# Performance work log

Hardware: AMD Instinct MI355X
Metric: run time of the kernel (lower is better)

## Reference

```python
import jax, jax.numpy as jnp
import numpy as np

N, IN_CH, HID, HEADS, OUT_CH, E = 30000, 256, 128, 4, 256, 480000
NEG_SLOPE = 0.2  # PyG GATConv default LeakyReLU slope


def setup_inputs() -> dict:
    key = jax.random.key(0)
    ks = jax.random.split(key, 12)
    s = lambda fin: 1.0 / np.sqrt(fin)
    return {
        "x": jax.random.normal(ks[0], (N, IN_CH), jnp.float32),
        "edge_index": jax.random.randint(ks[1], (2, E), 0, N, jnp.int32),
        "W1": jax.random.normal(ks[2], (IN_CH, HEADS * HID), jnp.float32) * s(IN_CH),
        "a_src1": jax.random.normal(ks[3], (HEADS, HID), jnp.float32) * s(HID),
        "a_dst1": jax.random.normal(ks[4], (HEADS, HID), jnp.float32) * s(HID),
        "b1": jnp.zeros((HEADS * HID,), jnp.float32),
        "prelu_w": jnp.asarray(0.25, jnp.float32),
        "W2": jax.random.normal(ks[5], (HEADS * HID, OUT_CH), jnp.float32) * s(HEADS * HID),
        "a_src2": jax.random.normal(ks[6], (1, OUT_CH), jnp.float32) * s(OUT_CH),
        "a_dst2": jax.random.normal(ks[7], (1, OUT_CH), jnp.float32) * s(OUT_CH),
        "b2": jnp.zeros((OUT_CH,), jnp.float32),
    }


def gat_conv(x, W, a_src, a_dst, bias, src, dst, heads, out_ch, concat):
    n = x.shape[0]
    h = (x @ W).reshape(n, heads, out_ch)                 # [n,H,C]
    al_s = jnp.einsum("nhc,hc->nh", h, a_src)             # [n,H]
    al_d = jnp.einsum("nhc,hc->nh", h, a_dst)
    logits = jax.nn.leaky_relu(al_s[src] + al_d[dst], NEG_SLOPE)  # [Et,H]
    m = jax.lax.stop_gradient(jax.ops.segment_max(logits, dst, num_segments=n))
    e = jnp.exp(logits - m[dst])
    denom = jax.ops.segment_sum(e, dst, num_segments=n)
    alpha = e / denom[dst]                                # per-dst softmax
    msg = h[src] * alpha[:, :, None]                      # [Et,H,C]
    out = jax.ops.segment_sum(msg, dst, num_segments=n)   # [n,H,C]
    out = out.reshape(n, heads * out_ch) if concat else out.mean(axis=1)
    return out + bias


def reference(x, edge_index, W1, a_src1, a_dst1, b1, prelu_w, W2, a_src2, a_dst2, b2):
    n = x.shape[0]
    loop = jnp.arange(n, dtype=edge_index.dtype)
    src = jnp.concatenate([edge_index[0], loop])          # PyG adds self-loops
    dst = jnp.concatenate([edge_index[1], loop])
    h = gat_conv(x, W1, a_src1, a_dst1, b1, src, dst, HEADS, HID, concat=True)
    h = jnp.where(h >= 0, h, prelu_w * h)                 # PReLU (eval: dropout off)
    z = gat_conv(h, W2, a_src2, a_dst2, b2, src, dst, 1, OUT_CH, concat=False)
    return z
```

## Files before the change

kernel.cpp:

```cpp
#include <hip/hip_runtime.h>
#include <hip/hip_bf16.h>
#include <float.h>

#define N_NODES 30000
#define IN_CH   256
#define HID     128
#define HEADS   4
#define OUT_CH  256
#define N_EDGES 480000
#define TOT_E   (N_EDGES + N_NODES)

typedef unsigned short u16;
typedef __attribute__((ext_vector_type(8))) unsigned short u16x8;
typedef __attribute__((ext_vector_type(8))) short          s16x8;
typedef __attribute__((ext_vector_type(4))) float          f32x4;

__device__ inline float bf2f(u16 u) {
    union { unsigned int i; float f; } v; v.i = ((unsigned int)u) << 16; return v.f;
}
__device__ inline u16 f2bf(float f) {
    union { float f; unsigned int i; } u; u.f = f;
    unsigned int r = u.i + 0x7FFF + ((u.i >> 16) & 1);
    return (u16)(r >> 16);
}

__global__ void detect_k(const unsigned int* __restrict__ w, int* __restrict__ flag) {
    __shared__ int votes;
    if (threadIdx.x == 0) votes = 0;
    __syncthreads();
    int v = 0;
    for (int i = threadIdx.x; i < 2048; i += 256) {
        unsigned int e = (w[i] >> 7) & 0xFFu;
        if (e >= 100u && e <= 140u) v++;
    }
    atomicAdd(&votes, v);
    __syncthreads();
    if (threadIdx.x == 0) *flag = (votes > 1024) ? 1 : 0;
}

__global__ void convert_bf_k(const void* __restrict__ in, u16* __restrict__ out,
                             int n, const int* __restrict__ flag) {
    int i = blockIdx.x * blockDim.x + threadIdx.x;
    if (i >= n) return;
    if (*flag) out[i] = ((const u16*)in)[i];
    else       out[i] = f2bf(((const float*)in)[i]);
}

__global__ void convert_tr_k(const void* __restrict__ in, u16* __restrict__ out,
                             int rows, int cols, const int* __restrict__ flag) {
    int i = blockIdx.x * blockDim.x + threadIdx.x;
    if (i >= rows * cols) return;
    int r = i / cols, c = i - r * cols;
    u16 v = (*flag) ? ((const u16*)in)[i] : f2bf(((const float*)in)[i]);
    out[(size_t)c * rows + r] = v;
}

__global__ void convert_small_k(const void* __restrict__ as1, const void* __restrict__ ad1,
                                const void* __restrict__ b1,  const void* __restrict__ as2,
                                const void* __restrict__ ad2, const void* __restrict__ b2,
                                const void* __restrict__ pw,
                                float* __restrict__ as1f, float* __restrict__ ad1f,
                                float* __restrict__ b1f,  float* __restrict__ as2f,
                                float* __restrict__ ad2f, float* __restrict__ b2f,
                                float* __restrict__ pwf,
                                const int* __restrict__ flag)
{
    int i = blockIdx.x * blockDim.x + threadIdx.x;
    int f = *flag;
#define CV(in, k) (f ? bf2f(((const u16*)(in))[k]) : ((const float*)(in))[k])
    if      (i < 512)  as1f[i]        = CV(as1, i);
    else if (i < 1024) ad1f[i - 512]  = CV(ad1, i - 512);
    else if (i < 1536) b1f [i - 1024] = CV(b1,  i - 1024);
    else if (i < 1792) as2f[i - 1536] = CV(as2, i - 1536);
    else if (i < 2048) ad2f[i - 1792] = CV(ad2, i - 1792);
    else if (i < 2304) b2f [i - 2048] = CV(b2,  i - 2048);
    else if (i == 2304) pwf[0]        = CV(pw, 0);
#undef CV
}

__global__ __launch_bounds__(256) void prep_av_k(
    const u16* __restrict__ W1t, const float* __restrict__ as1f,
    const float* __restrict__ ad1f, float* __restrict__ vsd)
{
    int idx = blockIdx.x * 256 + threadIdx.x;
    if (idx >= 2048) return;
    int v = idx >> 8;
    int k = idx & 255;
    int h = v & 3;
    const float* av = (v < 4) ? as1f : ad1f;
    float s = 0.f;
    for (int c = 0; c < 128; ++c)
        s += bf2f(W1t[(size_t)(h*128 + c)*256 + k]) * av[h*128 + c];
    vsd[idx] = s;
}

__global__ __launch_bounds__(64) void logits1_k(
    const u16* __restrict__ xb, const float* __restrict__ vsd,
    float* __restrict__ als, float* __restrict__ ald)
{
    int n = blockIdx.x, lane = threadIdx.x;
    int c0 = lane * 4;
    ushort4 xv = *(const ushort4*)(xb + (size_t)n*IN_CH + c0);
    float x0 = bf2f(xv.x), x1 = bf2f(xv.y), x2 = bf2f(xv.z), x3 = bf2f(xv.w);
#pragma unroll
    for (int v = 0; v < 8; ++v) {
        float4 vv = *(const float4*)(vsd + v*256 + c0);
        float d = x0*vv.x + x1*vv.y + x2*vv.z + x3*vv.w;
#pragma unroll
        for (int o = 32; o > 0; o >>= 1) d += __shfl_xor(d, o);
        if (lane == 0) {
            if (v < 4) als[(size_t)n*4 + v]     = d;
            else       ald[(size_t)n*4 + v - 4] = d;
        }
    }
}

__global__ __launch_bounds__(256) void gemm_bf_k(const u16* __restrict__ A,
                                                 const u16* __restrict__ Bt,
                                                 u16* __restrict__ Cb,
                                                 const float* __restrict__ a_s,
                                                 const float* __restrict__ a_d,
                                                 float* __restrict__ als,
                                                 float* __restrict__ ald,
                                                 int M, int N, int K,
                                                 int H, int hshift)
{
    __shared__ __align__(16) u16 As[128][40];
    __shared__ __align__(16) u16 Bs[128][40];

    const int tid  = threadIdx.x;
    const int wid  = tid >> 6;
    const int lane = tid & 63;
    const int wr   = wid >> 1;
    const int wc   = wid & 1;
    const int lr   = lane & 15;
    const int lg   = lane >> 4;
    const int row0 = blockIdx.y * 128;
    const int col0 = blockIdx.x * 128;

    const int st_r = tid >> 1;
    const int st_c = (tid & 1) << 4;

    f32x4 acc[4][4];
#pragma unroll
    for (int i = 0; i < 4; ++i)
#pragma unroll
        for (int j = 0; j < 4; ++j)
            acc[i][j] = (f32x4){0.f, 0.f, 0.f, 0.f};

    for (int k0 = 0; k0 < K; k0 += 32) {
        __syncthreads();
        {
            u16x8 a0 = {}, a1 = {};
            int ar = row0 + st_r;
            if (ar < M) {
                const u16* ap = A + (size_t)ar * K + k0 + st_c;
                a0 = *(const u16x8*)ap;
                a1 = *(const u16x8*)(ap + 8);
            }
            *(u16x8*)&As[st_r][st_c]     = a0;
            *(u16x8*)&As[st_r][st_c + 8] = a1;
            const u16* bp = Bt + (size_t)(col0 + st_r) * K + k0 + st_c;
            *(u16x8*)&Bs[st_r][st_c]     = *(const u16x8*)bp;
            *(u16x8*)&Bs[st_r][st_c + 8] = *(const u16x8*)(bp + 8);
        }
        __syncthreads();

        s16x8 af[4], bf[4];
#pragma unroll
        for (int mf = 0; mf < 4; ++mf)
            af[mf] = *(const s16x8*)&As[wr*64 + mf*16 + lr][lg*8];
#pragma unroll
        for (int nf = 0; nf < 4; ++nf)
            bf[nf] = *(const s16x8*)&Bs[wc*64 + nf*16 + lr][lg*8];
#pragma unroll
        for (int mf = 0; mf < 4; ++mf)
#pragma unroll
            for (int nf = 0; nf < 4; ++nf)
                acc[mf][nf] = __builtin_amdgcn_mfma_f32_16x16x32_bf16(
                    af[mf], bf[nf], acc[mf][nf], 0, 0, 0);
    }

    const int head = (col0 + wc*64) >> hshift;
    float asj[4], adj[4];
#pragma unroll
    for (int nf = 0; nf < 4; ++nf) {
        int j = col0 + wc*64 + nf*16 + lr;
        asj[nf] = a_s[j];
        adj[nf] = a_d[j];
    }
#pragma unroll
    for (int mf = 0; mf < 4; ++mf) {
#pragma unroll
        for (int r = 0; r < 4; ++r) {
            int rr = row0 + wr*64 + mf*16 + lg*4 + r;
            float ss = 0.f, sd = 0.f;
#pragma unroll
            for (int nf = 0; nf < 4; ++nf) {
                float v = acc[mf][nf][r];
                ss += v * asj[nf];
                sd += v * adj[nf];
            }
#pragma unroll
            for (int m2 = 1; m2 < 16; m2 <<= 1) {
                ss += __shfl_xor(ss, m2);
                sd += __shfl_xor(sd, m2);
            }
            if (rr < M) {
                if (lr == 0) {
                    atomicAdd(&als[(size_t)rr * H + head], ss);
                    atomicAdd(&ald[(size_t)rr * H + head], sd);
                }
                size_t base = (size_t)rr * N + col0 + wc*64 + lr;
#pragma unroll
                for (int nf = 0; nf < 4; ++nf)
                    Cb[base + nf*16] = f2bf(acc[mf][nf][r]);
            }
        }
    }
}

__global__ __launch_bounds__(256) void gemm_h1_k(const u16* __restrict__ A,
                                                 const u16* __restrict__ Bt,
                                                 u16* __restrict__ Cb,
                                                 const float* __restrict__ bias,
                                                 const float* __restrict__ prelu_w,
                                                 int M)
{
    __shared__ __align__(16) u16 As[128][40];
    __shared__ __align__(16) u16 Bs[128][40];

    const int h    = blockIdx.z;
    const int tid  = threadIdx.x;
    const int wid  = tid >> 6;
    const int lane = tid & 63;
    const int wr   = wid >> 1;
    const int wc   = wid & 1;
    const int lr   = lane & 15;
    const int lg   = lane >> 4;
    const int row0 = blockIdx.y * 128;

    const int st_r = tid >> 1;
    const int st_c = (tid & 1) << 4;

    f32x4 acc[4][4];
#pragma unroll
    for (int i = 0; i < 4; ++i)
#pragma unroll
        for (int j = 0; j < 4; ++j)
            acc[i][j] = (f32x4){0.f, 0.f, 0.f, 0.f};

    for (int k0 = 0; k0 < 256; k0 += 32) {
        __syncthreads();
        {
            u16x8 a0 = {}, a1 = {};
            int ar = row0 + st_r;
            if (ar < M) {
                const u16* ap = A + (size_t)ar * 1024 + h*256 + k0 + st_c;
                a0 = *(const u16x8*)ap;
                a1 = *(const u16x8*)(ap + 8);
            }
            *(u16x8*)&As[st_r][st_c]     = a0;
            *(u16x8*)&As[st_r][st_c + 8] = a1;
            const u16* bp = Bt + (size_t)(h*128 + st_r) * 256 + k0 + st_c;
            *(u16x8*)&Bs[st_r][st_c]     = *(const u16x8*)bp;
            *(u16x8*)&Bs[st_r][st_c + 8] = *(const u16x8*)(bp + 8);
        }
        __syncthreads();

        s16x8 af[4], bf[4];
#pragma unroll
        for (int mf = 0; mf < 4; ++mf)
            af[mf] = *(const s16x8*)&As[wr*64 + mf*16 + lr][lg*8];
#pragma unroll
        for (int nf = 0; nf < 4; ++nf)
            bf[nf] = *(const s16x8*)&Bs[wc*64 + nf*16 + lr][lg*8];
#pragma unroll
        for (int mf = 0; mf < 4; ++mf)
#pragma unroll
            for (int nf = 0; nf < 4; ++nf)
                acc[mf][nf] = __builtin_amdgcn_mfma_f32_16x16x32_bf16(
                    af[mf], bf[nf], acc[mf][nf], 0, 0, 0);
    }

    const float pw = *prelu_w;
#pragma unroll
    for (int mf = 0; mf < 4; ++mf) {
#pragma unroll
        for (int r = 0; r < 4; ++r) {
            int rr = row0 + wr*64 + mf*16 + lg*4 + r;
            if (rr >= M) continue;
            size_t base = (size_t)rr * 512 + h*128 + wc*64 + lr;
#pragma unroll
            for (int nf = 0; nf < 4; ++nf) {
                int j = wc*64 + nf*16 + lr;
                float v = acc[mf][nf][r] + bias[h*128 + j];
                v = (v >= 0.f) ? v : pw * v;
                Cb[base + nf*16] = f2bf(v);
            }
        }
    }
}

__global__ void zero_k(int* p, int n) {
    int i = blockIdx.x*blockDim.x + threadIdx.x; if (i < n) p[i] = 0;
}
__global__ void count_k(const int* __restrict__ ei, int* __restrict__ cnt) {
    int i = blockIdx.x*blockDim.x + threadIdx.x;
    if (i >= TOT_E) return;
    int d = (i < N_EDGES) ? ei[N_EDGES + i] : (i - N_EDGES);
    atomicAdd(&cnt[d], 1);
}
__global__ __launch_bounds__(1024) void scan1_k(const int* __restrict__ cnt,
                                                int* __restrict__ offs,
                                                int* __restrict__ btot)
{
    __shared__ int sm[1024];
    int tid = threadIdx.x;
    int i = blockIdx.x * 1024 + tid;
    int v = (i < N_NODES) ? cnt[i] : 0;
    sm[tid] = v;
    __syncthreads();
    for (int off = 1; off < 1024; off <<= 1) {
        int t = (tid >= off) ? sm[tid - off] : 0;
        __syncthreads();
        sm[tid] += t;
        __syncthreads();
    }
    if (i < N_NODES) offs[i + 1] = sm[tid];
    if (tid == 1023) btot[blockIdx.x] = sm[1023];
}
__global__ void scan2_k(const int* __restrict__ btot, int* __restrict__ bpref, int nb)
{
    int lane = threadIdx.x;
    int orig = (lane < nb) ? btot[lane] : 0;
    int v = orig;
    for (int off = 1; off < 64; off <<= 1) {
        int t = __shfl_up(v, off);
        if (lane >= off) v += t;
    }
    if (lane < nb) bpref[lane] = v - orig;
}
__global__ __launch_bounds__(1024) void scan3_k(const int* __restrict__ cnt,
                                                int* __restrict__ offs,
                                                int* __restrict__ cursor,
                                                const int* __restrict__ bpref)
{
    int i = blockIdx.x * 1024 + threadIdx.x;
    if (i < N_NODES) {
        int inc = offs[i + 1] + bpref[blockIdx.x];
        offs[i + 1] = inc;
        cursor[i]   = inc - cnt[i];
    }
    if (i == 0) offs[0] = 0;
}
__global__ void scatter_k(const int* __restrict__ ei, int* __restrict__ cursor,
                          int* __restrict__ ssrc)
{
    int i = blockIdx.x*blockDim.x + threadIdx.x;
    if (i >= TOT_E) return;
    int s, d;
    if (i < N_EDGES) { s = ei[i]; d = ei[N_EDGES + i]; }
    else             { s = i - N_EDGES; d = s; }
    int pos = atomicAdd(&cursor[d], 1);
    ssrc[pos] = s;
}

__global__ __launch_bounds__(64) void aggx_k(
    const u16* __restrict__ xb,
    const float* __restrict__ als,
    const float* __restrict__ ald,
    const int* __restrict__ offs,
    const int* __restrict__ ssrc,
    u16* __restrict__ aggx)
{
    const int n = blockIdx.x, tid = threadIdx.x;
    const int beg = offs[n], end = offs[n+1];

    float aldh[4];
#pragma unroll
    for (int h = 0; h < 4; ++h) aldh[h] = ald[(size_t)n*4 + h];

    float lsum[4] = {0.f, 0.f, 0.f, 0.f};
    for (int e = beg + tid; e < end; e += 64) {
        int s = ssrc[e];
        float4 a = *(const float4*)(als + (size_t)s*4);
        float la[4] = {a.x, a.y, a.z, a.w};
#pragma unroll
        for (int h = 0; h < 4; ++h) {
            float l = la[h] + aldh[h];
            l = (l >= 0.f) ? l : 0.2f*l;
            lsum[h] += __expf(l);
        }
    }
#pragma unroll
    for (int h = 0; h < 4; ++h)
#pragma unroll
        for (int o = 32; o > 0; o >>= 1) lsum[h] += __shfl_xor(lsum[h], o);
    float inv[4];
#pragma unroll
    for (int h = 0; h < 4; ++h) inv[h] = 1.0f / lsum[h];

    __shared__ int    sh_s[64];
    __shared__ float4 sh_w[64];
    const int c0 = tid * 4;
    float acc[4][4] = {};
    for (int chunk = beg; chunk < end; chunk += 64) {
        int e = chunk + tid;
        if (e < end) {
            int s = ssrc[e];
            sh_s[tid] = s;
            float4 a = *(const float4*)(als + (size_t)s*4);
            float la[4] = {a.x, a.y, a.z, a.w};
            float wv[4];
#pragma unroll
            for (int h = 0; h < 4; ++h) {
                float l = la[h] + aldh[h];
                l = (l >= 0.f) ? l : 0.2f*l;
                wv[h] = __expf(l) * inv[h];
            }
            sh_w[tid] = make_float4(wv[0], wv[1], wv[2], wv[3]);
        }
        __syncthreads();
        int cnt = min(64, end - chunk);
        int j = 0;
        for (; j + 4 <= cnt; j += 4) {
            int s0 = sh_s[j+0], s1 = sh_s[j+1], s2 = sh_s[j+2], s3 = sh_s[j+3];
            float4 w0 = sh_w[j+0], w1 = sh_w[j+1], w2 = sh_w[j+2], w3 = sh_w[j+3];
            ushort4 v0 = *(const ushort4*)(xb + (size_t)s0*IN_CH + c0);
            ushort4 v1 = *(const ushort4*)(xb + (size_t)s1*IN_CH + c0);
            ushort4 v2 = *(const ushort4*)(xb + (size_t)s2*IN_CH + c0);
            ushort4 v3 = *(const ushort4*)(xb + (size_t)s3*IN_CH + c0);
            float x0[4] = {bf2f(v0.x), bf2f(v0.y), bf2f(v0.z), bf2f(v0.w)};
            float x1[4] = {bf2f(v1.x), bf2f(v1.y), bf2f(v1.z), bf2f(v1.w)};
            float x2[4] = {bf2f(v2.x), bf2f(v2.y), bf2f(v2.z), bf2f(v2.w)};
            float x3[4] = {bf2f(v3.x), bf2f(v3.y), bf2f(v3.z), bf2f(v3.w)};
            float wa0[4] = {w0.x, w0.y, w0.z, w0.w};
            float wa1[4] = {w1.x, w1.y, w1.z, w1.w};
            float wa2[4] = {w2.x, w2.y, w2.z, w2.w};
            float wa3[4] = {w3.x, w3.y, w3.z, w3.w};
#pragma unroll
            for (int h = 0; h < 4; ++h)
#pragma unroll
                for (int k = 0; k < 4; ++k)
                    acc[h][k] += wa0[h]*x0[k] + wa1[h]*x1[k]
                               + wa2[h]*x2[k] + wa3[h]*x3[k];
        }
        for (; j < cnt; ++j) {
            int s0 = sh_s[j];
            float4 w0 = sh_w[j];
            ushort4 v0 = *(const ushort4*)(xb + (size_t)s0*IN_CH + c0);
            float x0[4] = {bf2f(v0.x), bf2f(v0.y), bf2f(v0.z), bf2f(v0.w)};
            float wa[4] = {w0.x, w0.y, w0.z, w0.w};
#pragma unroll
            for (int h = 0; h < 4; ++h)
#pragma unroll
                for (int k = 0; k < 4; ++k)
                    acc[h][k] += wa[h]*x0[k];
        }
        __syncthreads();
    }

    u16* op = aggx + (size_t)n * 1024;
#pragma unroll
    for (int h = 0; h < 4; ++h) {
        ushort4 o;
        o.x = f2bf(acc[h][0]); o.y = f2bf(acc[h][1]);
        o.z = f2bf(acc[h][2]); o.w = f2bf(acc[h][3]);
        *(ushort4*)(op + h*256 + c0) = o;
    }
}

template<int H, int C, int VW, bool PRELU, int OUTMODE>
__global__ __launch_bounds__(64) void aggregate_k(
    const u16* __restrict__ hb,
    const float* __restrict__ als,
    const float* __restrict__ ald,
    const int* __restrict__ offs,
    const int* __restrict__ ssrc,
    const float* __restrict__ bias,
    const float* __restrict__ prelu_w,
    void* __restrict__ outv,
    const int* __restrict__ flag)
{
    constexpr int CT = H * C;
    constexpr int T  = 64;
    static_assert(CT == T * VW, "geometry");
    const int n   = blockIdx.x;
    const int tid = threadIdx.x;
    const int beg = offs[n], end = offs[n+1];

    float aldh[H];
#pragma unroll
    for (int h = 0; h < H; ++h) aldh[h] = ald[(size_t)n*H + h];

    float lsum[H];
#pragma unroll
    for (int h = 0; h < H; ++h) lsum[h] = 0.f;
    for (int e = beg + tid; e < end; e += T) {
        int s = ssrc[e];
#pragma unroll
        for (int h = 0; h < H; ++h) {
            float l = als[(size_t)s*H + h] + aldh[h];
            l = (l >= 0.f) ? l : 0.2f*l;
            lsum[h] += __expf(l);
        }
    }
#pragma unroll
    for (int h = 0; h < H; ++h) {
#pragma unroll
        for (int o = 32; o > 0; o >>= 1) lsum[h] += __shfl_xor(lsum[h], o);
    }
    float inv[H];
#pragma unroll
    for (int h = 0; h < H; ++h) inv[h] = 1.0f / lsum[h];

    __shared__ int   sh_s[T];
    __shared__ float sh_w[H][T];
    const int hh = (VW * tid) / C;
    float acc[VW];
#pragma unroll
    for (int k = 0; k < VW; ++k) acc[k] = 0.f;

    for (int chunk = beg; chunk < end; chunk += T) {
        int e = chunk + tid;
        if (e < end) {
            int s = ssrc[e];
            sh_s[tid] = s;
#pragma unroll
            for (int h = 0; h < H; ++h) {
                float l = als[(size_t)s*H + h] + aldh[h];
                l = (l >= 0.f) ? l : 0.2f*l;
                sh_w[h][tid] = __expf(l) * inv[h];
            }
        }
        __syncthreads();
        int cnt = min(T, end - chunk);
        int j = 0;
        for (; j + 4 <= cnt; j += 4) {
            int   s0 = sh_s[j+0], s1 = sh_s[j+1], s2 = sh_s[j+2], s3 = sh_s[j+3];
            float w0 = sh_w[hh][j+0], w1 = sh_w[hh][j+1];
            float w2 = sh_w[hh][j+2], w3 = sh_w[hh][j+3];
            if constexpr (VW == 8) {
                u16x8 v0 = *(const u16x8*)(hb + (size_t)s0*CT + VW*tid);
                u16x8 v1 = *(const u16x8*)(hb + (size_t)s1*CT + VW*tid);
                u16x8 v2 = *(const u16x8*)(hb + (size_t)s2*CT + VW*tid);
                u16x8 v3 = *(const u16x8*)(hb + (size_t)s3*CT + VW*tid);
#pragma unroll
                for (int k = 0; k < 8; ++k) {
                    acc[k] += w0*bf2f(v0[k]) + w1*bf2f(v1[k])
                            + w2*bf2f(v2[k]) + w3*bf2f(v3[k]);
                }
            } else {
                ushort4 v0 = *(const ushort4*)(hb + (size_t)s0*CT + VW*tid);
                ushort4 v1 = *(const ushort4*)(hb + (size_t)s1*CT + VW*tid);
                ushort4 v2 = *(const ushort4*)(hb + (size_t)s2*CT + VW*tid);
                ushort4 v3 = *(const ushort4*)(hb + (size_t)s3*CT + VW*tid);
                acc[0] += w0*bf2f(v0.x) + w1*bf2f(v1.x) + w2*bf2f(v2.x) + w3*bf2f(v3.x);
                acc[1] += w0*bf2f(v0.y) + w1*bf2f(v1.y) + w2*bf2f(v2.y) + w3*bf2f(v3.y);
                acc[2] += w0*bf2f(v0.z) + w1*bf2f(v1.z) + w2*bf2f(v2.z) + w3*bf2f(v3.z);
                acc[3] += w0*bf2f(v0.w) + w1*bf2f(v1.w) + w2*bf2f(v2.w) + w3*bf2f(v3.w);
            }
        }
        for (; j < cnt; ++j) {
            int s0 = sh_s[j];
            float w0 = sh_w[hh][j];
            if constexpr (VW == 8) {
                u16x8 v0 = *(const u16x8*)(hb + (size_t)s0*CT + VW*tid);
#pragma unroll
                for (int k = 0; k < 8; ++k) acc[k] += w0*bf2f(v0[k]);
            } else {
                ushort4 v0 = *(const ushort4*)(hb + (size_t)s0*CT + VW*tid);
                acc[0] += w0*bf2f(v0.x); acc[1] += w0*bf2f(v0.y);
                acc[2] += w0*bf2f(v0.z); acc[3] += w0*bf2f(v0.w);
            }
        }
        __syncthreads();
    }

#pragma unroll
    for (int k = 0; k < VW; ++k) acc[k] += bias[VW*tid + k];
    if (PRELU) {
        float pw = *prelu_w;
#pragma unroll
        for (int k = 0; k < VW; ++k) acc[k] = (acc[k] >= 0.f) ? acc[k] : pw*acc[k];
    }
    size_t ofs = (size_t)n*CT + VW*tid;
    bool bf = (OUTMODE == 1) || (OUTMODE == 2 && *flag);
    if (bf) {
        if constexpr (VW == 8) {
            u16x8 o;
#pragma unroll
            for (int k = 0; k < 8; ++k) o[k] = f2bf(acc[k]);
            *(u16x8*)((u16*)outv + ofs) = o;
        } else {
            ushort4 o; o.x=f2bf(acc[0]); o.y=f2bf(acc[1]); o.z=f2bf(acc[2]); o.w=f2bf(acc[3]);
            *(ushort4*)((u16*)outv + ofs) = o;
        }
    } else {
        float* op = (float*)outv + ofs;
#pragma unroll
        for (int k = 0; k < VW; k += 4)
            *(float4*)(op + k) = make_float4(acc[k], acc[k+1], acc[k+2], acc[k+3]);
    }
}

extern "C" void kernel_launch(void* const* d_in, const int* in_sizes, int n_in,
                              void* d_out, int out_size, void* d_ws, size_t ws_size,
                              hipStream_t stream)
{
    const void* x   = d_in[0];
    const int*  ei  = (const int*)d_in[1];
    const void* W1  = d_in[2];
    const void* as1 = d_in[3];
    const void* ad1 = d_in[4];
    const void* b1  = d_in[5];
    const void* pw  = d_in[6];
    const void* W2  = d_in[7];
    const void* as2 = d_in[8];
    const void* ad2 = d_in[9];
    const void* b2  = d_in[10];

    float* ws = (float*)d_ws;
    int*   flag = (int*)ws;
    float* as1f = ws + 16;
    float* ad1f = as1f + 512;
    float* b1f  = ad1f + 512;
    float* as2f = b1f  + 512;
    float* ad2f = as2f + 256;
    float* b2f  = ad2f + 256;
    float* pwf  = b2f  + 256;
    float* vsd  = pwf + 16;
    u16*   W1t  = (u16*)(vsd + 2048);
    u16*   W2t  = W1t + IN_CH*HEADS*HID;
    float* als1 = (float*)(W2t + HEADS*HID*OUT_CH);
    float* ald1 = als1 + (size_t)N_NODES*HEADS;
    float* als2v = ald1 + (size_t)N_NODES*HEADS;
    float* ald2v = als2v + N_NODES;
    int*   cnt    = (int*)(ald2v + N_NODES);
    int*   offs   = cnt + N_NODES;
    int*   cursor = offs + 30004;
    int*   btot   = cursor + N_NODES;
    int*   bpref  = btot + 32;
    int*   ssrc   = bpref + 36;
    u16*   xb     = (u16*)(ssrc + 510004);
    u16*   aggx   = xb + (size_t)N_NODES*IN_CH;
    u16*   h1pb   = aggx + (size_t)N_NODES*1024;
    u16*   h2b    = aggx;

    const int NB = (N_NODES + 1023) / 1024;

    detect_k<<<1, 256, 0, stream>>>((const unsigned int*)x, flag);
    convert_bf_k<<<(N_NODES*IN_CH+255)/256, 256, 0, stream>>>(x, xb, N_NODES*IN_CH, flag);
    convert_tr_k<<<(IN_CH*HEADS*HID+255)/256, 256, 0, stream>>>(W1, W1t, IN_CH, HEADS*HID, flag);
    convert_tr_k<<<(HEADS*HID*OUT_CH+255)/256, 256, 0, stream>>>(W2, W2t, HEADS*HID, OUT_CH, flag);
    convert_small_k<<<10, 256, 0, stream>>>(as1, ad1, b1, as2, ad2, b2, pw,
                                            as1f, ad1f, b1f, as2f, ad2f, b2f, pwf, flag);
    prep_av_k<<<8, 256, 0, stream>>>(W1t, as1f, ad1f, vsd);

    zero_k<<<(90000+255)/256, 256, 0, stream>>>((int*)als2v, 90000);

    count_k  <<<(TOT_E+255)/256, 256, 0, stream>>>(ei, cnt);
    scan1_k  <<<NB, 1024, 0, stream>>>(cnt, offs, btot);
    scan2_k  <<<1, 64, 0, stream>>>(btot, bpref, NB);
    scan3_k  <<<NB, 1024, 0, stream>>>(cnt, offs, cursor, bpref);
    scatter_k<<<(TOT_E+255)/256, 256, 0, stream>>>(ei, cursor, ssrc);

    logits1_k<<<N_NODES, 64, 0, stream>>>(xb, vsd, als1, ald1);
    aggx_k<<<N_NODES, 64, 0, stream>>>(xb, als1, ald1, offs, ssrc, aggx);
    dim3 gh1(1, (N_NODES+127)/128, HEADS);
    gemm_h1_k<<<gh1, 256, 0, stream>>>(aggx, W1t, h1pb, b1f, pwf, N_NODES);

    dim3 g2(256/128, (N_NODES+127)/128);
    gemm_bf_k<<<g2, 256, 0, stream>>>(h1pb, W2t, h2b, as2f, ad2f, als2v, ald2v,
                                      N_NODES, OUT_CH, HEADS*HID, 1, 8);
    aggregate_k<1, OUT_CH, 4, false, 2>
        <<<N_NODES, 64, 0, stream>>>(h2b, als2v, ald2v, offs, ssrc, b2f, nullptr, d_out, flag);
}
```

Measured before the change: 349.5 us.

## Fuse x conversion into logits kernel and merge small weight-prep launches

Merges the W1/W2 transposed conversions, small parameter conversions and zeroing into one multi-role kernel, removing several launches. Folds the x fp32→bf16 conversion into the layer-1 logit kernel so x is read once and written as bf16 while the attention logits are computed. That kernel also packs 4 nodes per 256-thread block instead of one 64-thread block per node. The saving is one full pass over x plus launch overhead.

```diff
diff --git a/kernel.cpp b/kernel.cpp
--- a/kernel.cpp
+++ b/kernel.cpp
@@ -38,44 +38,46 @@
     if (threadIdx.x == 0) *flag = (votes > 1024) ? 1 : 0;
 }
 
-__global__ void convert_bf_k(const void* __restrict__ in, u16* __restrict__ out,
-                             int n, const int* __restrict__ flag) {
-    int i = blockIdx.x * blockDim.x + threadIdx.x;
-    if (i >= n) return;
-    if (*flag) out[i] = ((const u16*)in)[i];
-    else       out[i] = f2bf(((const float*)in)[i]);
-}
-
-__global__ void convert_tr_k(const void* __restrict__ in, u16* __restrict__ out,
-                             int rows, int cols, const int* __restrict__ flag) {
-    int i = blockIdx.x * blockDim.x + threadIdx.x;
-    if (i >= rows * cols) return;
-    int r = i / cols, c = i - r * cols;
-    u16 v = (*flag) ? ((const u16*)in)[i] : f2bf(((const float*)in)[i]);
-    out[(size_t)c * rows + r] = v;
-}
-
-__global__ void convert_small_k(const void* __restrict__ as1, const void* __restrict__ ad1,
-                                const void* __restrict__ b1,  const void* __restrict__ as2,
-                                const void* __restrict__ ad2, const void* __restrict__ b2,
-                                const void* __restrict__ pw,
-                                float* __restrict__ as1f, float* __restrict__ ad1f,
-                                float* __restrict__ b1f,  float* __restrict__ as2f,
-                                float* __restrict__ ad2f, float* __restrict__ b2f,
-                                float* __restrict__ pwf,
-                                const int* __restrict__ flag)
-{
-    int i = blockIdx.x * blockDim.x + threadIdx.x;
+__global__ void wconv_k(const void* __restrict__ W1, const void* __restrict__ W2,
+                        const void* __restrict__ as1, const void* __restrict__ ad1,
+                        const void* __restrict__ b1,  const void* __restrict__ as2,
+                        const void* __restrict__ ad2, const void* __restrict__ b2,
+                        const void* __restrict__ pw,
+                        u16* __restrict__ W1t, u16* __restrict__ W2t,
+                        float* __restrict__ as1f, float* __restrict__ ad1f,
+                        float* __restrict__ b1f,  float* __restrict__ as2f,
+                        float* __restrict__ ad2f, float* __restrict__ b2f,
+                        float* __restrict__ pwf,
+                        int* __restrict__ zeroreg,
+                        const int* __restrict__ flag)
+{
+    int b = blockIdx.x, t = threadIdx.x;
     int f = *flag;
+    if (b < 512) {
+        int idx = b*256 + t;
+        int r = idx >> 9, c = idx & 511;
+        u16 v = f ? ((const u16*)W1)[idx] : f2bf(((const float*)W1)[idx]);
+        W1t[(size_t)c*256 + r] = v;
+    } else if (b < 1024) {
+        int idx = (b-512)*256 + t;
+        int r = idx >> 8, c = idx & 255;
+        u16 v = f ? ((const u16*)W2)[idx] : f2bf(((const float*)W2)[idx]);
+        W2t[(size_t)c*512 + r] = v;
+    } else if (b < 1034) {
+        int i = (b-1024)*256 + t;
 #define CV(in, k) (f ? bf2f(((const u16*)(in))[k]) : ((const float*)(in))[k])
-    if      (i < 512)  as1f[i]        = CV(as1, i);
-    else if (i < 1024) ad1f[i - 512]  = CV(ad1, i - 512);
-    else if (i < 1536) b1f [i - 1024] = CV(b1,  i - 1024);
-    else if (i < 1792) as2f[i - 1536] = CV(as2, i - 1536);
-    else if (i < 2048) ad2f[i - 1792] = CV(ad2, i - 1792);
-    else if (i < 2304) b2f [i - 2048] = CV(b2,  i - 2048);
-    else if (i == 2304) pwf[0]        = CV(pw, 0);
+        if      (i < 512)  as1f[i]        = CV(as1, i);
+        else if (i < 1024) ad1f[i - 512]  = CV(ad1, i - 512);
+        else if (i < 1536) b1f [i - 1024] = CV(b1,  i - 1024);
+        else if (i < 1792) as2f[i - 1536] = CV(as2, i - 1536);
+        else if (i < 2048) ad2f[i - 1792] = CV(ad2, i - 1792);
+        else if (i < 2304) b2f [i - 2048] = CV(b2,  i - 2048);
+        else if (i == 2304) pwf[0]        = CV(pw, 0);
 #undef CV
+    } else {
+        int i = (b-1034)*256 + t;
+        if (i < 90000) zeroreg[i] = 0;
+    }
 }
 
 __global__ __launch_bounds__(256) void prep_av_k(
@@ -94,20 +96,32 @@
     vsd[idx] = s;
 }
 
-__global__ __launch_bounds__(64) void logits1_k(
-    const u16* __restrict__ xb, const float* __restrict__ vsd,
-    float* __restrict__ als, float* __restrict__ ald)
-{
-    int n = blockIdx.x, lane = threadIdx.x;
+__global__ __launch_bounds__(256) void xprep_k(
+    const void* __restrict__ x, const float* __restrict__ vsd,
+    u16* __restrict__ xb, float* __restrict__ als, float* __restrict__ ald,
+    const int* __restrict__ flag)
+{
+    int n = blockIdx.x * 4 + (threadIdx.x >> 6);
+    int lane = threadIdx.x & 63;
+    if (n >= N_NODES) return;
     int c0 = lane * 4;
-    ushort4 xv = *(const ushort4*)(xb + (size_t)n*IN_CH + c0);
-    float x0 = bf2f(xv.x), x1 = bf2f(xv.y), x2 = bf2f(xv.z), x3 = bf2f(xv.w);
+    u16 xr[4];
+    if (*flag) {
+        ushort4 v = *(const ushort4*)((const u16*)x + (size_t)n*IN_CH + c0);
+        xr[0]=v.x; xr[1]=v.y; xr[2]=v.z; xr[3]=v.w;
+    } else {
+        float4 v = *(const float4*)((const float*)x + (size_t)n*IN_CH + c0);
+        xr[0]=f2bf(v.x); xr[1]=f2bf(v.y); xr[2]=f2bf(v.z); xr[3]=f2bf(v.w);
+    }
+    ushort4 o; o.x=xr[0]; o.y=xr[1]; o.z=xr[2]; o.w=xr[3];
+    *(ushort4*)(xb + (size_t)n*IN_CH + c0) = o;
+    float x0=bf2f(xr[0]), x1=bf2f(xr[1]), x2=bf2f(xr[2]), x3=bf2f(xr[3]);
 #pragma unroll
     for (int v = 0; v < 8; ++v) {
         float4 vv = *(const float4*)(vsd + v*256 + c0);
         float d = x0*vv.x + x1*vv.y + x2*vv.z + x3*vv.w;
 #pragma unroll
-        for (int o = 32; o > 0; o >>= 1) d += __shfl_xor(d, o);
+        for (int o2 = 32; o2 > 0; o2 >>= 1) d += __shfl_xor(d, o2);
         if (lane == 0) {
             if (v < 4) als[(size_t)n*4 + v]     = d;
             else       ald[(size_t)n*4 + v - 4] = d;
@@ -302,9 +316,6 @@
     }
 }
 
-__global__ void zero_k(int* p, int n) {
-    int i = blockIdx.x*blockDim.x + threadIdx.x; if (i < n) p[i] = 0;
-}
 __global__ void count_k(const int* __restrict__ ei, int* __restrict__ cnt) {
     int i = blockIdx.x*blockDim.x + threadIdx.x;
     if (i >= TOT_E) return;
@@ -651,14 +662,10 @@
     const int NB = (N_NODES + 1023) / 1024;
 
     detect_k<<<1, 256, 0, stream>>>((const unsigned int*)x, flag);
-    convert_bf_k<<<(N_NODES*IN_CH+255)/256, 256, 0, stream>>>(x, xb, N_NODES*IN_CH, flag);
-    convert_tr_k<<<(IN_CH*HEADS*HID+255)/256, 256, 0, stream>>>(W1, W1t, IN_CH, HEADS*HID, flag);
-    convert_tr_k<<<(HEADS*HID*OUT_CH+255)/256, 256, 0, stream>>>(W2, W2t, HEADS*HID, OUT_CH, flag);
-    convert_small_k<<<10, 256, 0, stream>>>(as1, ad1, b1, as2, ad2, b2, pw,
-                                            as1f, ad1f, b1f, as2f, ad2f, b2f, pwf, flag);
+    wconv_k<<<1386, 256, 0, stream>>>(W1, W2, as1, ad1, b1, as2, ad2, b2, pw,
+                                      W1t, W2t, as1f, ad1f, b1f, as2f, ad2f, b2f, pwf,
+                                      (int*)als2v, flag);
     prep_av_k<<<8, 256, 0, stream>>>(W1t, as1f, ad1f, vsd);
-
-    zero_k<<<(90000+255)/256, 256, 0, stream>>>((int*)als2v, 90000);
 
     count_k  <<<(TOT_E+255)/256, 256, 0, stream>>>(ei, cnt);
     scan1_k  <<<NB, 1024, 0, stream>>>(cnt, offs, btot);
@@ -666,7 +673,7 @@
     scan3_k  <<<NB, 1024, 0, stream>>>(cnt, offs, cursor, bpref);
     scatter_k<<<(TOT_E+255)/256, 256, 0, stream>>>(ei, cursor, ssrc);
 
-    logits1_k<<<N_NODES, 64, 0, stream>>>(xb, vsd, als1, ald1);
+    xprep_k<<<(N_NODES+3)/4, 256, 0, stream>>>(x, vsd, xb, als1, ald1, flag);
     aggx_k<<<N_NODES, 64, 0, stream>>>(xb, als1, ald1, offs, ssrc, aggx);
     dim3 gh1(1, (N_NODES+127)/128, HEADS);
     gemm_h1_k<<<gh1, 256, 0, stream>>>(aggx, W1t, h1pb, b1f, pwf, N_NODES);
```

Result: faster. 334.6 us (-4.3%).
